# Optimization experiments

Measured on AMD Instinct MI355X. Metric: run time of the kernel, lower is better.

The kernel has to match this reference:

```python
import jax, jax.numpy as jnp
import numpy as np

B, H, N, T = 16, 16, 4096, 8
D_S, D_ID, L, K = 256, 128, 8, 32
HS, DQ = 8, 32
D_HID = 1024
D_STEER = 3 * D_S + D_ID  # cat(s_cur, id_cur, walker_state, token_embed)


def _gelu(x):
    return jax.nn.gelu(x, approximate=False)


def _rms(x, w):
    return x * jax.lax.rsqrt(jnp.mean(x * x, axis=-1, keepdims=True) + 1e-6) * w


def _mlp2(x, w1, b1, w2, b2):
    return _gelu(x @ w1 + b1) @ w2 + b2


def _per_plane_mlp(x, plane_idx, W1, b1, W2, b2):
    # x: [n, D_in]; plane_idx: [n] int in [0,L). Vectorized plane dispatch:
    # compute all planes then select (avoids data-dependent masking).
    h_all = jnp.einsum('nd,phd->nph', x, W1) + b1[None]          # [n,L,D_hid]
    h = jnp.take_along_axis(h_all, plane_idx[:, None, None], axis=1)[:, 0]
    h = _gelu(h)
    o_all = jnp.einsum('nh,pdh->npd', h, W2) + b2[None]          # [n,L,D_out]
    return jnp.take_along_axis(o_all, plane_idx[:, None, None], axis=1)[:, 0]


def setup_inputs() -> dict:
    key = jax.random.key(0)
    ks = jax.random.split(key, 16)
    f = jax.random.normal
    return {
        's': f(ks[0], (B, N, D_S), jnp.float32),
        'node_id': f(ks[1], (N, D_ID), jnp.float32),
        'walker_state': f(ks[2], (B, H, D_S), jnp.float32),
        'token_embed': f(ks[3], (B, T, D_S), jnp.float32),
        'norm_w': jnp.ones((D_S,), jnp.float32),
        'W1': f(ks[4], (L, D_HID, D_STEER), jnp.float32) * 0.014,
        'b1': jnp.zeros((L, D_HID), jnp.float32),
        'W2': f(ks[5], (L, D_S, D_HID), jnp.float32) * (2.0 / D_HID) ** 0.5,
        'b2': jnp.zeros((L, D_S), jnp.float32),
        'qw1': f(ks[6], (D_STEER, 2 * HS * DQ), jnp.float32) * 0.014,
        'qb1': jnp.zeros((2 * HS * DQ,), jnp.float32),
        'qw2': f(ks[7], (2 * HS * DQ, HS * DQ), jnp.float32) * 0.02,
        'qb2': jnp.zeros((HS * DQ,), jnp.float32),
        'kw1': f(ks[8], (D_ID, 2 * HS * DQ), jnp.float32) * 0.014,
        'kb1': jnp.zeros((2 * HS * DQ,), jnp.float32),
        'kw2': f(ks[9], (2 * HS * DQ, HS * DQ), jnp.float32) * 0.02,
        'kb2': jnp.zeros((HS * DQ,), jnp.float32),
        'walker_pos': jax.random.randint(ks[10], (B, H), 0, N, jnp.int32),
        'plane_idx': jax.random.randint(ks[11], (B, H), 0, L, jnp.int32),
        'neighbors': jax.random.randint(ks[12], (N, K), 0, N, jnp.int32),
    }


def reference(s, node_id, walker_state, token_embed, norm_w, W1, b1, W2, b2,
              qw1, qb1, qw2, qb2, kw1, kb1, kw2, kb2,
              walker_pos, plane_idx, neighbors):
    b_idx = jnp.arange(B)[:, None]            # [B,1] batch gather index
    plane_flat = plane_idx.reshape(-1)        # [B*H], constant per walker
    scale = 1.0 / (HS * np.sqrt(DQ).astype(np.float32))

    def step(carry, tok):
        s, pos, wstate, co, vc, lb = carry
        s_cur = s[b_idx, pos]                 # gather [B,H,D_s]
        id_cur = node_id[pos]                 # [B,H,D_id]
        s_n = _rms(s_cur, norm_w)
        tok_b = jnp.broadcast_to(tok[:, None, :], (B, H, D_S))
        steer = jnp.concatenate([s_n, id_cur, wstate, tok_b], axis=-1)  # [B,H,D_steer]
        # per-plane content MLP (dispatch by plane index)
        content = _per_plane_mlp(steer.reshape(B * H, D_STEER), plane_flat,
                                 W1, b1, W2, b2).reshape(B, H, D_S)
        # shared q/k projections and neighbor scoring
        q = _mlp2(steer, qw1, qb1, qw2, qb2).reshape(B, H, HS, DQ)
        nbr = neighbors[pos]                  # [B,H,K]
        k = _mlp2(node_id[nbr], kw1, kb1, kw2, kb2).reshape(B, H, K, HS, DQ)
        scores = jnp.einsum('bhsd,bhksd->bhk', q, k) * scale   # [B,H,K]
        probs = jax.nn.softmax(scores, axis=-1)
        mp = probs.mean(axis=(0, 1))
        lb = lb + K * jnp.sum(mp * mp)        # load-balance penalty
        # non-differentiable hop: argmax move
        sel = jnp.argmax(scores, axis=-1)     # [B,H]
        next_pos = jnp.take_along_axis(nbr, sel[..., None], axis=-1)[..., 0]
        # state updates: scatter content into s, residual walker state
        s_new = s.at[b_idx, pos].add(content)
        wstate_new = wstate + content
        # non-grad co-visit / visit-count accumulators
        pf = pos.reshape(-1)
        nf = next_pos.reshape(-1)
        co = co.at[pf, nf].add(1.0)
        vc = vc.at[nf].add(1.0)
        motor = wstate_new.mean(axis=1)       # [B,D_s]
        return (s_new, next_pos, wstate_new, co, vc, lb), motor

    init = (s, walker_pos, walker_state,
            jnp.zeros((N, N), jnp.float32), jnp.zeros((N,), jnp.float32),
            jnp.float32(0.0))
    (s_new, pos_new, ws_new, co, vc, lb), motors = jax.lax.scan(
        step, init, token_embed.transpose(1, 0, 2))
    motor_bt = motors.transpose(1, 0, 2)      # [B,T,D_s]
    return motor_bt, s_new, pos_new, ws_new, co, vc, lb
```

## Files before the change

kernel.cpp:

```cpp
#include <hip/hip_runtime.h>
#include <math.h>

#define B_    16
#define H_    16
#define N_    4096
#define T_    8
#define DS_   256
#define DID_  128
#define L_    8
#define K_    32
#define DHID_ 1024
#define DSTEER_ 896
#define QH_   512
#define QO_   256
#define NW_   256
#define SLOTS_ 512
#define SCORE_SCALE 0.022097086912079608f

struct KArgs {
    const float *s_in, *node_id, *ws_in, *token, *norm_w;
    const float *W1, *b1, *W2, *b2;
    const float *qw1, *qb1, *qw2, *qb2, *kw1, *kb1, *kw2, *kb2;
    const int *walker_pos, *plane_idx, *neighbors;
    float *out_motor, *out_s, *out_pos, *out_ws, *out_co, *out_vc, *out_lb;
    float *keys, *kh, *steer, *steerT, *h1p, *q1p, *c2p, *q2p, *mp_all;
    int *pos, *plane_order, *chunk_plane, *chunk_rows, *slot_of, *nchunks;
};

__device__ __forceinline__ float gelu_exact(float x) {
    return 0.5f * x * (1.0f + erff(x * 0.70710678118654752f));
}

#define FMA4(c, b, a) { c.x = fmaf(b.x, (a), c.x); c.y = fmaf(b.y, (a), c.y); \
                        c.z = fmaf(b.z, (a), c.z); c.w = fmaf(b.w, (a), c.w); }

__device__ __forceinline__ void gelu4(float4& v) {
    v.x = gelu_exact(v.x); v.y = gelu_exact(v.y);
    v.z = gelu_exact(v.z); v.w = gelu_exact(v.w);
}

__device__ __forceinline__ void rgemm_inner(
    const float* __restrict__ a0, const float* __restrict__ a1,
    const float* bp, int ldb, int K,
    float4& c0, float4& c1)
{
    for (int k = 0; k < K; k += 8) {
        const float4 a0l = *reinterpret_cast<const float4*>(a0 + k);
        const float4 a0h = *reinterpret_cast<const float4*>(a0 + k + 4);
        const float4 a1l = *reinterpret_cast<const float4*>(a1 + k);
        const float4 a1h = *reinterpret_cast<const float4*>(a1 + k + 4);
        const float* b8 = bp + (size_t)k * ldb;
#define KSTEP(o, av0, av1) { float4 bv = *reinterpret_cast<const float4*>(b8 + (size_t)(o) * ldb); \
                             FMA4(c0, bv, av0); FMA4(c1, bv, av1); }
        KSTEP(0, a0l.x, a1l.x)
        KSTEP(1, a0l.y, a1l.y)
        KSTEP(2, a0l.z, a1l.z)
        KSTEP(3, a0l.w, a1l.w)
        KSTEP(4, a0h.x, a1h.x)
        KSTEP(5, a0h.y, a1h.y)
        KSTEP(6, a0h.z, a1h.z)
        KSTEP(7, a0h.w, a1h.w)
#undef KSTEP
    }
}


__global__ __launch_bounds__(256) void setup1_kernel(KArgs a)
{
    int bid = blockIdx.x, tid = threadIdx.x;
    if (bid < 1024) {
        int u = bid;
        int rt = u >> 3, ct = u & 7;
        int tr = tid >> 4, tc = tid & 15;
        int row = rt * 32 + tr * 2, col = ct * 64 + tc * 4;
        const float* a0 = a.node_id + (size_t)row * DID_;
        float4 c0 = {0.f,0.f,0.f,0.f}, c1 = {0.f,0.f,0.f,0.f};
        rgemm_inner(a0, a0 + DID_, a.kw1 + col, QH_, DID_, c0, c1);
        float4 bv = *reinterpret_cast<const float4*>(a.kb1 + col);
        c0.x += bv.x; c0.y += bv.y; c0.z += bv.z; c0.w += bv.w;
        c1.x += bv.x; c1.y += bv.y; c1.z += bv.z; c1.w += bv.w;
        gelu4(c0); gelu4(c1);
        *reinterpret_cast<float4*>(a.kh + (size_t)row * QH_ + col) = c0;
        *reinterpret_cast<float4*>(a.kh + (size_t)(row + 1) * QH_ + col) = c1;
    } else if (bid == 1024) {
        a.pos[tid] = a.walker_pos[tid];
        a.mp_all[tid] = 0.f;
        __shared__ int cnt_s[8];
        __shared__ int cplane_s[16], cbase_s[16];
        __shared__ int nch_s;
        int wave = tid >> 6, lane = tid & 63;
        for (int pp = wave; pp < 8; pp += 4) {
            int base = 0;
            for (int c0 = 0; c0 < NW_; c0 += 64) {
                int w = c0 + lane;
                bool hit = (a.plane_idx[w] == pp);
                unsigned long long mask = __ballot(hit);
                if (hit) {
                    int rank = __popcll(mask & ((1ull << lane) - 1ull));
                    a.plane_order[pp * NW_ + base + rank] = w;
                }
                base += __popcll(mask);
            }
            if (lane == 0) cnt_s[pp] = base;
        }
        __syncthreads();
        if (tid == 0) {
            int nc = 0;
            for (int p = 0; p < 8; ++p)
                for (int s0 = 0; s0 < cnt_s[p]; s0 += 32) {
                    cplane_s[nc] = p; cbase_s[nc] = s0; ++nc;
                }
            *a.nchunks = nc;
            nch_s = nc;
        }
        __syncthreads();
        int nc = nch_s;
        for (int idx = tid; idx < 512; idx += 256) {
            int c = idx >> 5, i = idx & 31;
            int v = -1;
            if (c < nc) {
                int p = cplane_s[c];
                int r = cbase_s[c] + i;
                if (r < cnt_s[p]) v = a.plane_order[p * NW_ + r];
            }
            a.chunk_rows[c * 32 + i] = v;
            if (v >= 0) a.slot_of[v] = c * 32 + i;
            if (i == 0) a.chunk_plane[c] = (c < nc) ? cplane_s[c] : 0;
        }
    } else {
        int gid = (bid - 1025) * 256 + tid, stride = 4096 * 256;
        const float4 z = {0.f, 0.f, 0.f, 0.f};
        float4* co4 = reinterpret_cast<float4*>(a.out_co);
        float4* s4o = reinterpret_cast<float4*>(a.out_s);
        const float4* s4i = reinterpret_cast<const float4*>(a.s_in);
        for (int i = gid; i < 4194304; i += stride) co4[i] = z;
        for (int i = gid; i < 4194304; i += stride) s4o[i] = s4i[i];
        float4* m4 = reinterpret_cast<float4*>(a.out_motor);
        for (int i = gid; i < 8192; i += stride) m4[i] = z;
        float4* w4o = reinterpret_cast<float4*>(a.out_ws);
        const float4* w4i = reinterpret_cast<const float4*>(a.ws_in);
        for (int i = gid; i < 16384; i += stride) w4o[i] = w4i[i];
        float4* v4 = reinterpret_cast<float4*>(a.out_vc);
        for (int i = gid; i < 1024; i += stride) v4[i] = z;
        if (gid == 0) a.out_lb[0] = 0.f;
    }
}


__device__ void dev_steer(const KArgs& a, int w, int tid, int t) {
    int b = w >> 4;
    int p = a.pos[w];
    int slot = a.slot_of[w];
    float sc = a.out_s[((size_t)b * N_ + p) * DS_ + tid];
    float v = sc * sc;
    for (int off = 32; off > 0; off >>= 1) v += __shfl_down(v, off);
    __shared__ float red[4];
    if ((tid & 63) == 0) red[tid >> 6] = v;
    __syncthreads();
    float tot = red[0] + red[1] + red[2] + red[3];
    float r = rsqrtf(tot * (1.0f / DS_) + 1e-6f);
    float* st = a.steer + (size_t)w * DSTEER_;
    float v0 = sc * r * a.norm_w[tid];
    float v2 = a.out_ws[(size_t)w * DS_ + tid];
    float v3 = a.token[((size_t)b * T_ + t) * DS_ + tid];
    st[tid] = v0;
    st[384 + tid] = v2;
    st[640 + tid] = v3;
    a.steerT[(size_t)tid * SLOTS_ + slot] = v0;
    a.steerT[(size_t)(384 + tid) * SLOTS_ + slot] = v2;
    a.steerT[(size_t)(640 + tid) * SLOTS_ + slot] = v3;
    if (tid < 128) {
        float v1 = a.node_id[(size_t)p * DID_ + tid];
        st[256 + tid] = v1;
        a.steerT[(size_t)(256 + tid) * SLOTS_ + slot] = v1;
    }
}


__global__ __launch_bounds__(256) void setup2_kernel(KArgs a)
{
    int bid = blockIdx.x, tid = threadIdx.x;
    if (bid < 512) {
        int rt = bid >> 2, ct = bid & 3;
        int tr = tid >> 4, tc = tid & 15;
        int row = rt * 32 + tr * 2, col = ct * 64 + tc * 4;
        const float* a0 = a.kh + (size_t)row * QH_;
        float4 c0 = {0.f,0.f,0.f,0.f}, c1 = {0.f,0.f,0.f,0.f};
        rgemm_inner(a0, a0 + QH_, a.kw2 + col, QO_, QH_, c0, c1);
        float4 bv = *reinterpret_cast<const float4*>(a.kb2 + col);
        c0.x += bv.x; c0.y += bv.y; c0.z += bv.z; c0.w += bv.w;
        c1.x += bv.x; c1.y += bv.y; c1.z += bv.z; c1.w += bv.w;
        *reinterpret_cast<float4*>(a.keys + (size_t)row * QO_ + col) = c0;
        *reinterpret_cast<float4*>(a.keys + (size_t)(row + 1) * QO_ + col) = c1;
    } else {
        dev_steer(a, bid - 512, tid, 0);
    }
}

__global__ __launch_bounds__(256) void steer_kernel(KArgs a, int t)
{
    dev_steer(a, blockIdx.x, threadIdx.x, t);
}


__global__ __launch_bounds__(256) void l1_kernel(KArgs a)
{
    __shared__ float bs[112 * 64];
    int bid = blockIdx.x, tid = threadIdx.x;
    float4 c0 = {0.f,0.f,0.f,0.f}, c1 = {0.f,0.f,0.f,0.f};
    if (bid < 512) {
        int kp = bid & 7, tile = bid >> 3;
        int rt = tile >> 3, ct = tile & 7;
        int tr = tid >> 4, tc = tid & 15;
        int row = rt * 32 + tr * 2, col0 = ct * 64;
#pragma unroll
        for (int i = 0; i < 7; ++i) {
            int idx = tid + i * 256;
            int kk = idx >> 4, c4 = (idx & 15) << 2;
            *reinterpret_cast<float4*>(bs + kk * 64 + c4) =
                *reinterpret_cast<const float4*>(a.qw1 + (size_t)(kp * 112 + kk) * QH_ + col0 + c4);
        }
        __syncthreads();
        const float* a0 = a.steer + (size_t)row * DSTEER_ + kp * 112;
        rgemm_inner(a0, a0 + DSTEER_, bs + tc * 4, 64, 112, c0, c1);
        float* o = a.q1p + (size_t)kp * 131072;
        int col = col0 + tc * 4;
        *reinterpret_cast<float4*>(o + (size_t)row * QH_ + col) = c0;
        *reinterpret_cast<float4*>(o + (size_t)(row + 1) * QH_ + col) = c1;
    } else {
        int b2 = bid - 512;
        int kp = b2 & 7, tile = b2 >> 3;
        int c = tile >> 4, jt = tile & 15;
        if (c >= *a.nchunks) return;
        int p = a.chunk_plane[c];
        int tr = tid >> 3, tc = tid & 7;
        int J = jt * 64 + tr * 2;
#pragma unroll
        for (int i = 0; i < 4; ++i) {
            int idx = tid + i * 256;
            if (idx < 896) {
                int kk = idx >> 3, s4 = (idx & 7) << 2;
                *reinterpret_cast<float4*>(bs + kk * 32 + s4) =
                    *reinterpret_cast<const float4*>(a.steerT + (size_t)(kp * 112 + kk) * SLOTS_ + c * 32 + s4);
            }
        }
        __syncthreads();
        const float* a0 = a.W1 + ((size_t)p * DHID_ + J) * DSTEER_ + kp * 112;
        rgemm_inner(a0, a0 + DSTEER_, bs + tc * 4, 32, 112, c0, c1);
        float* o = a.h1p + (size_t)kp * 524288;
        int slot = c * 32 + tc * 4;
        *reinterpret_cast<float4*>(o + (size_t)J * SLOTS_ + slot) = c0;
        *reinterpret_cast<float4*>(o + (size_t)(J + 1) * SLOTS_ + slot) = c1;
    }
}


__global__ __launch_bounds__(256) void l2f_kernel(KArgs a)
{
    __shared__ float smem[4096];
    int bid = blockIdx.x, tid = threadIdx.x;
    if (bid < 256) {
        int kp = bid & 7, tile = bid >> 3;
        int rt = tile >> 2, ct = tile & 3;
        int tr = tid >> 4, tc = tid & 15;
        int row0 = rt * 32, col = ct * 64 + tc * 4;
        float4 c0 = {0.f,0.f,0.f,0.f}, c1 = {0.f,0.f,0.f,0.f};
#pragma unroll
        for (int i = 0; i < 2; ++i) {
            int idx = tid + i * 256;
            int r = idx >> 4, k4 = (idx & 15) << 2;
            size_t off = (size_t)(row0 + r) * QH_ + kp * 64 + k4;
            float4 acc = *reinterpret_cast<const float4*>(a.qb1 + kp * 64 + k4);
#pragma unroll
            for (int p8 = 0; p8 < 8; ++p8) {
                float4 v = *reinterpret_cast<const float4*>(a.q1p + (size_t)p8 * 131072 + off);
                acc.x += v.x; acc.y += v.y; acc.z += v.z; acc.w += v.w;
            }
            gelu4(acc);
            *reinterpret_cast<float4*>(smem + r * 72 + k4) = acc;
        }
        __syncthreads();
        const float* a0 = smem + (tr * 2) * 72;
        rgemm_inner(a0, a0 + 72, a.qw2 + (size_t)(kp * 64) * QO_ + col, QO_, 64, c0, c1);
        float* o = a.q2p + (size_t)kp * 65536;
        int row = row0 + tr * 2;
        *reinterpret_cast<float4*>(o + (size_t)row * QO_ + col) = c0;
        *reinterpret_cast<float4*>(o + (size_t)(row + 1) * QO_ + col) = c1;
    } else {
        int b2i = bid - 256;
        int kp = b2i & 7, tile = b2i >> 3;
        int c = tile >> 2, jt = tile & 3;
        if (c >= *a.nchunks) return;
        int p = a.chunk_plane[c];
        int tr = tid >> 3, tc = tid & 7;
        int J = jt * 64 + tr * 2;
        float4 c0 = {0.f,0.f,0.f,0.f}, c1 = {0.f,0.f,0.f,0.f};
#pragma unroll
        for (int i = 0; i < 4; ++i) {
            int idx = tid + i * 256;
            int kk = idx >> 3, s4 = (idx & 7) << 2;
            int kq = kp * 128 + kk;
            size_t off = (size_t)kq * SLOTS_ + c * 32 + s4;
            float bj = a.b1[p * DHID_ + kq];
            float4 acc = {bj, bj, bj, bj};
#pragma unroll
            for (int p8 = 0; p8 < 8; ++p8) {
                float4 v = *reinterpret_cast<const float4*>(a.h1p + (size_t)p8 * 524288 + off);
                acc.x += v.x; acc.y += v.y; acc.z += v.z; acc.w += v.w;
            }
            gelu4(acc);
            *reinterpret_cast<float4*>(smem + kk * 32 + s4) = acc;
        }
        __syncthreads();
        const float* a0 = a.W2 + ((size_t)p * DS_ + J) * DHID_ + kp * 128;
        rgemm_inner(a0, a0 + DHID_, smem + tc * 4, 32, 128, c0, c1);
        float* o = a.c2p + (size_t)kp * 131072;
        int slot = c * 32 + tc * 4;
        *reinterpret_cast<float4*>(o + (size_t)J * SLOTS_ + slot) = c0;
        *reinterpret_cast<float4*>(o + (size_t)(J + 1) * SLOTS_ + slot) = c1;
    }
}


__global__ __launch_bounds__(256) void score_kernel(KArgs a, int t)
{
    int w = blockIdx.x;
    int b = w >> 4;
    int tid = threadIdx.x;
    int pold = a.pos[w];
    int slot = a.slot_of[w];
    __shared__ float qv_s[256];
    __shared__ int nbr_s[32];
    __shared__ float part_s[8][32];
    __shared__ float sc_s[32];
    if (tid < 32) nbr_s[tid] = a.neighbors[(size_t)pold * K_ + tid];
    float qsum = a.qb2[tid];
#pragma unroll
    for (int kp = 0; kp < 8; ++kp) qsum += a.q2p[(size_t)kp * 65536 + (size_t)w * QO_ + tid];
    qv_s[tid] = qsum;
    float csum = a.b2[a.chunk_plane[slot >> 5] * DS_ + tid];
#pragma unroll
    for (int kp = 0; kp < 8; ++kp) csum += a.c2p[(size_t)kp * 131072 + (size_t)tid * SLOTS_ + slot];
    __syncthreads();
    int k = tid & 31, part = tid >> 5;
    int nk = nbr_s[k];
    const float* kp_ = a.keys + (size_t)nk * 256 + part * 32;
    const float* qp = qv_s + part * 32;
    float acc = 0.f;
#pragma unroll
    for (int i = 0; i < 32; i += 4) {
        float4 kv = *reinterpret_cast<const float4*>(kp_ + i);
        acc += kv.x * qp[i] + kv.y * qp[i+1] + kv.z * qp[i+2] + kv.w * qp[i+3];
    }
    part_s[part][k] = acc;
    __syncthreads();
    if (tid < 32) {
        float s = 0.f;
#pragma unroll
        for (int p8 = 0; p8 < 8; ++p8) s += part_s[p8][tid];
        sc_s[tid] = s * SCORE_SCALE;
    }
    __syncthreads();
    if (tid < 32) {
        float sv = sc_s[tid];
        float m = sv;
        for (int off = 1; off < 32; off <<= 1) m = fmaxf(m, __shfl_xor(m, off));
        float e = expf(sv - m);
        float ssum = e;
        for (int off = 1; off < 32; off <<= 1) ssum += __shfl_xor(ssum, off);
        float prob = e / ssum;
        atomicAdd(&a.mp_all[t * 32 + tid], prob);
        float bs = sv; int bi = tid;
        for (int off = 1; off < 32; off <<= 1) {
            float os = __shfl_xor(bs, off);
            int   oi = __shfl_xor(bi, off);
            if (os > bs || (os == bs && oi < bi)) { bs = os; bi = oi; }
        }
        if (tid == 0) {
            int next = nbr_s[bi];
            a.pos[w] = next;
            if (t == T_ - 1) a.out_pos[w] = (float)next;
            atomicAdd(&a.out_co[(size_t)pold * N_ + next], 1.0f);
            atomicAdd(&a.out_vc[next], 1.0f);
        }
    }
    atomicAdd(&a.out_s[((size_t)b * N_ + pold) * DS_ + tid], csum);
    float wn = a.out_ws[(size_t)w * DS_ + tid] + csum;
    a.out_ws[(size_t)w * DS_ + tid] = wn;
    atomicAdd(&a.out_motor[((size_t)b * T_ + t) * DS_ + tid], wn * (1.0f / H_));
}

__global__ __launch_bounds__(256) void final_kernel(KArgs a)
{
    int tid = threadIdx.x;
    float v = a.mp_all[tid] * (1.0f / 256.f);
    v = v * v;
    for (int off = 32; off > 0; off >>= 1) v += __shfl_down(v, off);
    __shared__ float red[4];
    if ((tid & 63) == 0) red[tid >> 6] = v;
    __syncthreads();
    if (tid == 0) a.out_lb[0] = (float)K_ * (red[0] + red[1] + red[2] + red[3]);
}


extern "C" void kernel_launch(void* const* d_in, const int* in_sizes, int n_in,
                              void* d_out, int out_size, void* d_ws, size_t ws_size,
                              hipStream_t stream)
{
    KArgs a;
    a.s_in    = (const float*)d_in[0];
    a.node_id = (const float*)d_in[1];
    a.ws_in   = (const float*)d_in[2];
    a.token   = (const float*)d_in[3];
    a.norm_w  = (const float*)d_in[4];
    a.W1  = (const float*)d_in[5];
    a.b1  = (const float*)d_in[6];
    a.W2  = (const float*)d_in[7];
    a.b2  = (const float*)d_in[8];
    a.qw1 = (const float*)d_in[9];
    a.qb1 = (const float*)d_in[10];
    a.qw2 = (const float*)d_in[11];
    a.qb2 = (const float*)d_in[12];
    a.kw1 = (const float*)d_in[13];
    a.kb1 = (const float*)d_in[14];
    a.kw2 = (const float*)d_in[15];
    a.kb2 = (const float*)d_in[16];
    a.walker_pos = (const int*)d_in[17];
    a.plane_idx  = (const int*)d_in[18];
    a.neighbors  = (const int*)d_in[19];

    float* out = (float*)d_out;
    a.out_motor = out;
    a.out_s     = a.out_motor + 32768;
    a.out_pos   = a.out_s + (size_t)16777216;
    a.out_ws    = a.out_pos + 256;
    a.out_co    = a.out_ws + 65536;
    a.out_vc    = a.out_co + (size_t)16777216;
    a.out_lb    = a.out_vc + 4096;

    float* ws = (float*)d_ws;
    a.keys   = ws;
    a.steer  = a.keys + 1048576;
    a.steerT = a.steer + 229376;
    a.h1p    = a.steerT + 458752;
    a.kh     = a.h1p;
    a.q1p    = a.h1p + 4194304;
    a.c2p    = a.q1p + 1048576;
    a.q2p    = a.c2p + 1048576;
    a.mp_all = a.q2p + 524288;
    a.pos         = (int*)(a.mp_all + 256);
    a.plane_order = a.pos + 256;
    a.chunk_plane = a.plane_order + 2048;
    a.chunk_rows  = a.chunk_plane + 16;
    a.slot_of     = a.chunk_rows + 512;
    a.nchunks     = a.slot_of + 256;

    setup1_kernel<<<1024 + 1 + 4096, 256, 0, stream>>>(a);
    setup2_kernel<<<512 + 256, 256, 0, stream>>>(a);
    for (int t = 0; t < T_; ++t) {
        l1_kernel<<<2560, 256, 0, stream>>>(a);
        l2f_kernel<<<768, 256, 0, stream>>>(a);
        score_kernel<<<256, 256, 0, stream>>>(a, t);
        if (t < T_ - 1) steer_kernel<<<256, 256, 0, stream>>>(a, t + 1);
    }
    final_kernel<<<1, 256, 0, stream>>>(a);
}
```

Measured before the change: 548.3 us.

## Transpose c2p partials to slot-major layout and move zero-fills to memset

The l2f kernel now stages its output tile through shared memory and writes c2p in slot-major order. The score kernel can then read each walker's 256 outputs contiguously instead of with a 512-float stride. The zeroing of co, vc, lb and motor moves out of setup1 into hipMemsetAsync calls, and setup1 launches half as many copy blocks. This adds an extra shared-memory round trip and two barriers in l2f. The single memset covering co, vc and lb relies on those buffers being contiguous in memory.

```diff
diff --git a/kernel.cpp b/kernel.cpp
--- a/kernel.cpp
+++ b/kernel.cpp
@@ -128,21 +128,13 @@
             if (i == 0) a.chunk_plane[c] = (c < nc) ? cplane_s[c] : 0;
         }
     } else {
-        int gid = (bid - 1025) * 256 + tid, stride = 4096 * 256;
-        const float4 z = {0.f, 0.f, 0.f, 0.f};
-        float4* co4 = reinterpret_cast<float4*>(a.out_co);
+        int gid = (bid - 1025) * 256 + tid, stride = 2048 * 256;
         float4* s4o = reinterpret_cast<float4*>(a.out_s);
         const float4* s4i = reinterpret_cast<const float4*>(a.s_in);
-        for (int i = gid; i < 4194304; i += stride) co4[i] = z;
         for (int i = gid; i < 4194304; i += stride) s4o[i] = s4i[i];
-        float4* m4 = reinterpret_cast<float4*>(a.out_motor);
-        for (int i = gid; i < 8192; i += stride) m4[i] = z;
         float4* w4o = reinterpret_cast<float4*>(a.out_ws);
         const float4* w4i = reinterpret_cast<const float4*>(a.ws_in);
         for (int i = gid; i < 16384; i += stride) w4o[i] = w4i[i];
-        float4* v4 = reinterpret_cast<float4*>(a.out_vc);
-        for (int i = gid; i < 1024; i += stride) v4[i] = z;
-        if (gid == 0) a.out_lb[0] = 0.f;
     }
 }
 
@@ -314,10 +306,29 @@
         __syncthreads();
         const float* a0 = a.W2 + ((size_t)p * DS_ + J) * DHID_ + kp * 128;
         rgemm_inner(a0, a0 + DHID_, smem + tc * 4, 32, 128, c0, c1);
+        __syncthreads();
+        int jl = tr * 2;
+        smem[(tc*4+0)*66 + jl]     = c0.x;
+        smem[(tc*4+1)*66 + jl]     = c0.y;
+        smem[(tc*4+2)*66 + jl]     = c0.z;
+        smem[(tc*4+3)*66 + jl]     = c0.w;
+        smem[(tc*4+0)*66 + jl + 1] = c1.x;
+        smem[(tc*4+1)*66 + jl + 1] = c1.y;
+        smem[(tc*4+2)*66 + jl + 1] = c1.z;
+        smem[(tc*4+3)*66 + jl + 1] = c1.w;
+        __syncthreads();
         float* o = a.c2p + (size_t)kp * 131072;
-        int slot = c * 32 + tc * 4;
-        *reinterpret_cast<float4*>(o + (size_t)J * SLOTS_ + slot) = c0;
-        *reinterpret_cast<float4*>(o + (size_t)(J + 1) * SLOTS_ + slot) = c1;
+#pragma unroll
+        for (int i = 0; i < 2; ++i) {
+            int f4i = tid + i * 256;
+            int sl = f4i >> 4, j4 = (f4i & 15) << 2;
+            float4 v;
+            v.x = smem[sl * 66 + j4 + 0];
+            v.y = smem[sl * 66 + j4 + 1];
+            v.z = smem[sl * 66 + j4 + 2];
+            v.w = smem[sl * 66 + j4 + 3];
+            *reinterpret_cast<float4*>(o + (size_t)(c * 32 + sl) * 256 + jt * 64 + j4) = v;
+        }
     }
 }
 
@@ -340,7 +351,7 @@
     qv_s[tid] = qsum;
     float csum = a.b2[a.chunk_plane[slot >> 5] * DS_ + tid];
 #pragma unroll
-    for (int kp = 0; kp < 8; ++kp) csum += a.c2p[(size_t)kp * 131072 + (size_t)tid * SLOTS_ + slot];
+    for (int kp = 0; kp < 8; ++kp) csum += a.c2p[(size_t)kp * 131072 + (size_t)slot * 256 + tid];
     __syncthreads();
     int k = tid & 31, part = tid >> 5;
     int nk = nbr_s[k];
@@ -455,7 +466,10 @@
     a.slot_of     = a.chunk_rows + 512;
     a.nchunks     = a.slot_of + 256;
 
-    setup1_kernel<<<1024 + 1 + 4096, 256, 0, stream>>>(a);
+    hipMemsetAsync(a.out_motor, 0, 32768 * sizeof(float), stream);
+    hipMemsetAsync(a.out_co, 0, (size_t)(16777216 + 4096 + 1) * sizeof(float), stream);
+
+    setup1_kernel<<<1024 + 1 + 2048, 256, 0, stream>>>(a);
     setup2_kernel<<<512 + 256, 256, 0, stream>>>(a);
     for (int t = 0; t < T_; ++t) {
         l1_kernel<<<2560, 256, 0, stream>>>(a);
```

Measured after the change: 512.8 us. 6.5% less time.
